# Kernel optimization log

Hardware: AMD Instinct MI355X
Metric: run time of the kernel (lower is better)

## Reference

```python
import jax, jax.numpy as jnp
import numpy as np

N, C = 131072, 1000
ALPHA_LINK = 0.25  # weight applied when pred is a 'linked' (acceptable) confusion of gt
GAMMA = 2.0        # focal exponent


def setup_inputs() -> dict:
    key = jax.random.key(0)
    k1, k2, k3, k4 = jax.random.split(key, 4)
    y_pred = jax.random.normal(k1, (N, C), dtype=jnp.float32)
    y_true = jax.random.randint(k2, (N,), 0, C, dtype=jnp.int64)
    # Dense representation of the python link dict: link_matrix[gt, pred] == True
    # iff pred is in link[gt]; has_link[gt] == True iff gt is a key of link.
    link_matrix = jax.random.bernoulli(k3, 0.01, (C, C))
    has_link = jax.random.bernoulli(k4, 0.5, (C,))
    return {"y_pred": y_pred, "y_true": y_true,
            "link_matrix": link_matrix, "has_link": has_link}


def reference(y_pred, y_true, link_matrix, has_link):
    # per-sample cross entropy (stable log-softmax + gather)
    logp = jax.nn.log_softmax(y_pred, axis=-1)                     # [N, C]
    ce = -jnp.take_along_axis(logp, y_true[:, None], axis=1)[:, 0]  # [N]
    pt = jnp.exp(-ce)                                              # [N]
    pred = jnp.argmax(y_pred, axis=1)                              # [N]
    # link_bad: ALPHA_LINK iff pred != gt, gt in link, and pred in link[gt]; else 1
    linked = link_matrix[y_true, pred] & has_link[y_true] & (pred != y_true)
    w = jnp.where(linked, jnp.float32(ALPHA_LINK), jnp.float32(1.0))
    return jnp.mean(w * (1.0 - pt) ** GAMMA * ce)
```

## Files before the change

### kernel.cpp

```cpp
#include <hip/hip_runtime.h>
#include <math.h>


#define NROWS 131072
#define NC 1000
#define NF4 250
#define ROWS_PER_WAVE 4
#define WAVES_PER_BLOCK 4
#define ROWS_PER_BLOCK (ROWS_PER_WAVE * WAVES_PER_BLOCK)
#define NBLOCKS (NROWS / ROWS_PER_BLOCK)
#define NWAVES (NBLOCKS * WAVES_PER_BLOCK)
#define ALPHA_LINK 0.25f

typedef float floatx4 __attribute__((ext_vector_type(4)));

__device__ __forceinline__ void load_row_nt(const floatx4* __restrict__ rowp,
                                            int lane, floatx4 v[4]) {
    v[0] = __builtin_nontemporal_load(rowp + lane);
    v[1] = __builtin_nontemporal_load(rowp + lane + 64);
    v[2] = __builtin_nontemporal_load(rowp + lane + 128);
    if (lane + 192 < NF4) v[3] = __builtin_nontemporal_load(rowp + lane + 192);
    else                  v[3] = (floatx4){-INFINITY, -INFINITY, -INFINITY, -INFINITY};
}

__device__ __forceinline__ void row_local(const floatx4 v[4], int lane, int tf, int tl,
                                          float& m, int& idx, float& xt, float& s) {
    m = -INFINITY; idx = 1 << 30; xt = 0.0f;
    #pragma unroll
    for (int k = 0; k < 4; ++k) {
        const int f  = lane + 64 * k;
        const int c0 = f * 4;
        const float x0 = v[k].x, x1 = v[k].y, x2 = v[k].z, x3 = v[k].w;
        if (x0 > m) { m = x0; idx = c0; }
        if (x1 > m) { m = x1; idx = c0 + 1; }
        if (x2 > m) { m = x2; idx = c0 + 2; }
        if (x3 > m) { m = x3; idx = c0 + 3; }
        if (f == tf) xt = (tl == 0) ? x0 : (tl == 1) ? x1 : (tl == 2) ? x2 : x3;
    }
    s = 0.0f;
    #pragma unroll
    for (int k = 0; k < 4; ++k) {
        s += __expf(v[k].x - m) + __expf(v[k].y - m)
           + __expf(v[k].z - m) + __expf(v[k].w - m);
    }
}

__global__ __launch_bounds__(256) void lfl_main(
    const float* __restrict__ yp,
    const int* __restrict__ yt,
    const unsigned char* __restrict__ linkb, const int* __restrict__ linki,
    const unsigned char* __restrict__ hasb,  const int* __restrict__ hasi,
    const unsigned int* __restrict__ hlw,
    float* __restrict__ partial)
{
    const int lane  = threadIdx.x & 63;
    const int wid   = threadIdx.x >> 6;
    const int gwave = blockIdx.x * WAVES_PER_BLOCK + wid;

    const int hi = yt[2 * lane + 1];
    const int y64 = (__ballot(hi != 0) == 0ULL);
    const unsigned int h0 = hlw[lane];
    const unsigned int h1 = hlw[lane + 64];
    const unsigned int h2 = hlw[lane + 128];
    const unsigned int h3 = (lane + 192 < NF4) ? hlw[lane + 192] : 0u;
    const int bfmt = (__ballot((h0 > 1u) | (h1 > 1u) | (h2 > 1u) | (h3 > 1u)) != 0ULL);

    const int row0 = blockIdx.x * ROWS_PER_BLOCK + wid * ROWS_PER_WAVE;
    float wsum = 0.0f;

    #pragma unroll
    for (int p = 0; p < ROWS_PER_WAVE / 2; ++p) {
        const int rowA = row0 + 2 * p;
        const int rowB = rowA + 1;

        floatx4 vA[4], vB[4];
        load_row_nt((const floatx4*)(yp + (size_t)rowA * NC), lane, vA);
        load_row_nt((const floatx4*)(yp + (size_t)rowB * NC), lane, vB);

        const int tgtA = y64 ? yt[2 * rowA] : yt[rowA];
        const int tgtB = y64 ? yt[2 * rowB] : yt[rowB];
        const int tfA = tgtA >> 2, tlA = tgtA & 3;
        const int tfB = tgtB >> 2, tlB = tgtB & 3;

        float mA, xtA, sA, mB, xtB, sB;
        int idxA, idxB;
        row_local(vA, lane, tfA, tlA, mA, idxA, xtA, sA);
        row_local(vB, lane, tfB, tlB, mB, idxB, xtB, sB);

        const float xtsA = __shfl(xtA, tfA & 63);
        const float xtsB = __shfl(xtB, tfB & 63);

        #pragma unroll
        for (int off = 32; off; off >>= 1) {
            const float omA = __shfl_xor(mA, off);
            const float omB = __shfl_xor(mB, off);
            const int   oiA = __shfl_xor(idxA, off);
            const int   oiB = __shfl_xor(idxB, off);
            const float osA = __shfl_xor(sA, off);
            const float osB = __shfl_xor(sB, off);
            const float mnA = fmaxf(mA, omA);
            const float mnB = fmaxf(mB, omB);
            sA = sA * __expf(mA - mnA) + osA * __expf(omA - mnA);
            sB = sB * __expf(mB - mnB) + osB * __expf(omB - mnB);
            if (omA > mA || (omA == mA && oiA < idxA)) idxA = oiA;
            if (omB > mB || (omB == mB && oiB < idxB)) idxB = oiB;
            mA = mnA; mB = mnB;
        }

        #pragma unroll
        for (int q = 0; q < 2; ++q) {
            const int   target = q ? tgtB : tgtA;
            const int   pred   = q ? idxB : idxA;
            const float logp_t = (q ? xtsB : xtsA) - (q ? mB : mA) - __logf(q ? sB : sA);
            const float ce = -logp_t;
            const float pt = __expf(logp_t);
            const size_t ofs = (size_t)target * NC + (size_t)pred;
            const bool lm = bfmt ? (linkb[ofs] != 0)   : (linki[ofs] != 0);
            const bool hb = bfmt ? (hasb[target] != 0) : (hasi[target] != 0);
            const float w = (lm && hb && (pred != target)) ? ALPHA_LINK : 1.0f;
            const float ompt = 1.0f - pt;
            wsum += w * ompt * ompt * ce;
        }
    }

    if (lane == 0) partial[gwave] = wsum;
}

__global__ __launch_bounds__(1024) void lfl_final(const float* __restrict__ partial,
                                                  float* __restrict__ out) {
    __shared__ float sm[1024];
    float s = 0.0f;
    for (int i = threadIdx.x; i < NWAVES; i += 1024) s += partial[i];
    sm[threadIdx.x] = s;
    __syncthreads();
    for (int stride = 512; stride; stride >>= 1) {
        if ((int)threadIdx.x < stride) sm[threadIdx.x] += sm[threadIdx.x + stride];
        __syncthreads();
    }
    if (threadIdx.x == 0) out[0] = sm[0] * (1.0f / (float)NROWS);
}

extern "C" void kernel_launch(void* const* d_in, const int* in_sizes, int n_in,
                              void* d_out, int out_size, void* d_ws, size_t ws_size,
                              hipStream_t stream) {
    const float* yp = (const float*)d_in[0];
    const int*   yt = (const int*)d_in[1];
    const void*  lk = d_in[2];
    const void*  hl = d_in[3];

    float* partial = (float*)d_ws;

    lfl_main<<<NBLOCKS, 256, 0, stream>>>(
        yp, yt,
        (const unsigned char*)lk, (const int*)lk,
        (const unsigned char*)hl, (const int*)hl,
        (const unsigned int*)hl,
        partial);
    lfl_final<<<1, 1024, 0, stream>>>(partial, (float*)d_out);
}
```

Before: 103.4 us.

## Double-buffer row-pair loads and process more rows per wave

Cuts the grid to 2048 blocks so each wave handles 16 rows. Row pairs are loaded through two alternating register buffers, so the loads for the next pair are in flight while the current pair computes. Targets are prefetched up front and launch bounds request 4 blocks per CU. This is meant to hide memory latency for a bandwidth-bound kernel, at the cost of higher register pressure and fewer waves to hide latency.

```diff
diff --git a/kernel.cpp b/kernel.cpp
--- a/kernel.cpp
+++ b/kernel.cpp
@@ -5,47 +5,107 @@
 #define NROWS 131072
 #define NC 1000
 #define NF4 250
-#define ROWS_PER_WAVE 4
 #define WAVES_PER_BLOCK 4
-#define ROWS_PER_BLOCK (ROWS_PER_WAVE * WAVES_PER_BLOCK)
-#define NBLOCKS (NROWS / ROWS_PER_BLOCK)
+#define NBLOCKS 2048
 #define NWAVES (NBLOCKS * WAVES_PER_BLOCK)
+#define ROWS_PER_WAVE (NROWS / NWAVES)
+#define NPAIRS (ROWS_PER_WAVE / 2)
 #define ALPHA_LINK 0.25f
 
 typedef float floatx4 __attribute__((ext_vector_type(4)));
 
-__device__ __forceinline__ void load_row_nt(const floatx4* __restrict__ rowp,
-                                            int lane, floatx4 v[4]) {
-    v[0] = __builtin_nontemporal_load(rowp + lane);
-    v[1] = __builtin_nontemporal_load(rowp + lane + 64);
-    v[2] = __builtin_nontemporal_load(rowp + lane + 128);
-    if (lane + 192 < NF4) v[3] = __builtin_nontemporal_load(rowp + lane + 192);
-    else                  v[3] = (floatx4){-INFINITY, -INFINITY, -INFINITY, -INFINITY};
+__device__ __forceinline__ void load_pair_nt(const float* __restrict__ yp,
+                                             int row, int lane, floatx4 v[2][4]) {
+    #pragma unroll
+    for (int r = 0; r < 2; ++r) {
+        const floatx4* rowp = (const floatx4*)(yp + (size_t)(row + r) * NC);
+        v[r][0] = __builtin_nontemporal_load(rowp + lane);
+        v[r][1] = __builtin_nontemporal_load(rowp + lane + 64);
+        v[r][2] = __builtin_nontemporal_load(rowp + lane + 128);
+        if (lane + 192 < NF4) v[r][3] = __builtin_nontemporal_load(rowp + lane + 192);
+        else v[r][3] = (floatx4){-INFINITY, -INFINITY, -INFINITY, -INFINITY};
+    }
 }
 
-__device__ __forceinline__ void row_local(const floatx4 v[4], int lane, int tf, int tl,
-                                          float& m, int& idx, float& xt, float& s) {
-    m = -INFINITY; idx = 1 << 30; xt = 0.0f;
+__device__ __forceinline__ float compute_pair(
+    const floatx4 v[2][4], int lane, int tgtA, int tgtB, int bfmt,
+    const unsigned char* __restrict__ linkb, const int* __restrict__ linki,
+    const unsigned char* __restrict__ hasb,  const int* __restrict__ hasi)
+{
+    const int tfA = tgtA >> 2, tlA = tgtA & 3;
+    const int tfB = tgtB >> 2, tlB = tgtB & 3;
+
+    float mA = -INFINITY, mB = -INFINITY, xtA = 0.0f, xtB = 0.0f;
+    int idxA = 1 << 30, idxB = 1 << 30;
     #pragma unroll
     for (int k = 0; k < 4; ++k) {
         const int f  = lane + 64 * k;
         const int c0 = f * 4;
-        const float x0 = v[k].x, x1 = v[k].y, x2 = v[k].z, x3 = v[k].w;
-        if (x0 > m) { m = x0; idx = c0; }
-        if (x1 > m) { m = x1; idx = c0 + 1; }
-        if (x2 > m) { m = x2; idx = c0 + 2; }
-        if (x3 > m) { m = x3; idx = c0 + 3; }
-        if (f == tf) xt = (tl == 0) ? x0 : (tl == 1) ? x1 : (tl == 2) ? x2 : x3;
+        {
+            const float x0 = v[0][k].x, x1 = v[0][k].y, x2 = v[0][k].z, x3 = v[0][k].w;
+            if (x0 > mA) { mA = x0; idxA = c0; }
+            if (x1 > mA) { mA = x1; idxA = c0 + 1; }
+            if (x2 > mA) { mA = x2; idxA = c0 + 2; }
+            if (x3 > mA) { mA = x3; idxA = c0 + 3; }
+            if (f == tfA) xtA = (tlA == 0) ? x0 : (tlA == 1) ? x1 : (tlA == 2) ? x2 : x3;
+        }
+        {
+            const float x0 = v[1][k].x, x1 = v[1][k].y, x2 = v[1][k].z, x3 = v[1][k].w;
+            if (x0 > mB) { mB = x0; idxB = c0; }
+            if (x1 > mB) { mB = x1; idxB = c0 + 1; }
+            if (x2 > mB) { mB = x2; idxB = c0 + 2; }
+            if (x3 > mB) { mB = x3; idxB = c0 + 3; }
+            if (f == tfB) xtB = (tlB == 0) ? x0 : (tlB == 1) ? x1 : (tlB == 2) ? x2 : x3;
+        }
     }
-    s = 0.0f;
+    float sA = 0.0f, sB = 0.0f;
     #pragma unroll
     for (int k = 0; k < 4; ++k) {
-        s += __expf(v[k].x - m) + __expf(v[k].y - m)
-           + __expf(v[k].z - m) + __expf(v[k].w - m);
+        sA += __expf(v[0][k].x - mA) + __expf(v[0][k].y - mA)
+            + __expf(v[0][k].z - mA) + __expf(v[0][k].w - mA);
+        sB += __expf(v[1][k].x - mB) + __expf(v[1][k].y - mB)
+            + __expf(v[1][k].z - mB) + __expf(v[1][k].w - mB);
     }
+
+    const float xtsA = __shfl(xtA, tfA & 63);
+    const float xtsB = __shfl(xtB, tfB & 63);
+
+    #pragma unroll
+    for (int off = 32; off; off >>= 1) {
+        const float omA = __shfl_xor(mA, off);
+        const float omB = __shfl_xor(mB, off);
+        const int   oiA = __shfl_xor(idxA, off);
+        const int   oiB = __shfl_xor(idxB, off);
+        const float osA = __shfl_xor(sA, off);
+        const float osB = __shfl_xor(sB, off);
+        const float mnA = fmaxf(mA, omA);
+        const float mnB = fmaxf(mB, omB);
+        sA = sA * __expf(mA - mnA) + osA * __expf(omA - mnA);
+        sB = sB * __expf(mB - mnB) + osB * __expf(omB - mnB);
+        if (omA > mA || (omA == mA && oiA < idxA)) idxA = oiA;
+        if (omB > mB || (omB == mB && oiB < idxB)) idxB = oiB;
+        mA = mnA; mB = mnB;
+    }
+
+    float wsum = 0.0f;
+    #pragma unroll
+    for (int q = 0; q < 2; ++q) {
+        const int   target = q ? tgtB : tgtA;
+        const int   pred   = q ? idxB : idxA;
+        const float logp_t = (q ? xtsB : xtsA) - (q ? mB : mA) - __logf(q ? sB : sA);
+        const float ce = -logp_t;
+        const float pt = __expf(logp_t);
+        const size_t ofs = (size_t)target * NC + (size_t)pred;
+        const bool lm = bfmt ? (linkb[ofs] != 0)   : (linki[ofs] != 0);
+        const bool hb = bfmt ? (hasb[target] != 0) : (hasi[target] != 0);
+        const float w = (lm && hb && (pred != target)) ? ALPHA_LINK : 1.0f;
+        const float ompt = 1.0f - pt;
+        wsum += w * ompt * ompt * ce;
+    }
+    return wsum;
 }
 
-__global__ __launch_bounds__(256) void lfl_main(
+__global__ __launch_bounds__(256, 4) void lfl_main(
     const float* __restrict__ yp,
     const int* __restrict__ yt,
     const unsigned char* __restrict__ linkb, const int* __restrict__ linki,
@@ -56,71 +116,40 @@
     const int lane  = threadIdx.x & 63;
     const int wid   = threadIdx.x >> 6;
     const int gwave = blockIdx.x * WAVES_PER_BLOCK + wid;
+    const int row0  = gwave * ROWS_PER_WAVE;
 
-    const int hi = yt[2 * lane + 1];
-    const int y64 = (__ballot(hi != 0) == 0ULL);
+    const int det_hi = yt[2 * lane + 1];
     const unsigned int h0 = hlw[lane];
     const unsigned int h1 = hlw[lane + 64];
     const unsigned int h2 = hlw[lane + 128];
     const unsigned int h3 = (lane + 192 < NF4) ? hlw[lane + 192] : 0u;
+    int t32[ROWS_PER_WAVE], t64[ROWS_PER_WAVE];
+    #pragma unroll
+    for (int r = 0; r < ROWS_PER_WAVE; ++r) {
+        t32[r] = yt[row0 + r];
+        t64[r] = yt[2 * (row0 + r)];
+    }
+
+    floatx4 A[2][4], B[2][4];
+    load_pair_nt(yp, row0, lane, A);
+
+    const int y64  = (__ballot(det_hi != 0) == 0ULL);
     const int bfmt = (__ballot((h0 > 1u) | (h1 > 1u) | (h2 > 1u) | (h3 > 1u)) != 0ULL);
 
-    const int row0 = blockIdx.x * ROWS_PER_BLOCK + wid * ROWS_PER_WAVE;
+    int tgt[ROWS_PER_WAVE];
+    #pragma unroll
+    for (int r = 0; r < ROWS_PER_WAVE; ++r) tgt[r] = y64 ? t64[r] : t32[r];
+
     float wsum = 0.0f;
-
     #pragma unroll
-    for (int p = 0; p < ROWS_PER_WAVE / 2; ++p) {
-        const int rowA = row0 + 2 * p;
-        const int rowB = rowA + 1;
-
-        floatx4 vA[4], vB[4];
-        load_row_nt((const floatx4*)(yp + (size_t)rowA * NC), lane, vA);
-        load_row_nt((const floatx4*)(yp + (size_t)rowB * NC), lane, vB);
-
-        const int tgtA = y64 ? yt[2 * rowA] : yt[rowA];
-        const int tgtB = y64 ? yt[2 * rowB] : yt[rowB];
-        const int tfA = tgtA >> 2, tlA = tgtA & 3;
-        const int tfB = tgtB >> 2, tlB = tgtB & 3;
-
-        float mA, xtA, sA, mB, xtB, sB;
-        int idxA, idxB;
-        row_local(vA, lane, tfA, tlA, mA, idxA, xtA, sA);
-        row_local(vB, lane, tfB, tlB, mB, idxB, xtB, sB);
-
-        const float xtsA = __shfl(xtA, tfA & 63);
-        const float xtsB = __shfl(xtB, tfB & 63);
-
-        #pragma unroll
-        for (int off = 32; off; off >>= 1) {
-            const float omA = __shfl_xor(mA, off);
-            const float omB = __shfl_xor(mB, off);
-            const int   oiA = __shfl_xor(idxA, off);
-            const int   oiB = __shfl_xor(idxB, off);
-            const float osA = __shfl_xor(sA, off);
-            const float osB = __shfl_xor(sB, off);
-            const float mnA = fmaxf(mA, omA);
-            const float mnB = fmaxf(mB, omB);
-            sA = sA * __expf(mA - mnA) + osA * __expf(omA - mnA);
-            sB = sB * __expf(mB - mnB) + osB * __expf(omB - mnB);
-            if (omA > mA || (omA == mA && oiA < idxA)) idxA = oiA;
-            if (omB > mB || (omB == mB && oiB < idxB)) idxB = oiB;
-            mA = mnA; mB = mnB;
-        }
-
-        #pragma unroll
-        for (int q = 0; q < 2; ++q) {
-            const int   target = q ? tgtB : tgtA;
-            const int   pred   = q ? idxB : idxA;
-            const float logp_t = (q ? xtsB : xtsA) - (q ? mB : mA) - __logf(q ? sB : sA);
-            const float ce = -logp_t;
-            const float pt = __expf(logp_t);
-            const size_t ofs = (size_t)target * NC + (size_t)pred;
-            const bool lm = bfmt ? (linkb[ofs] != 0)   : (linki[ofs] != 0);
-            const bool hb = bfmt ? (hasb[target] != 0) : (hasi[target] != 0);
-            const float w = (lm && hb && (pred != target)) ? ALPHA_LINK : 1.0f;
-            const float ompt = 1.0f - pt;
-            wsum += w * ompt * ompt * ce;
-        }
+    for (int p = 0; p < NPAIRS; p += 2) {
+        if (p + 1 < NPAIRS) load_pair_nt(yp, row0 + (p + 1) * 2, lane, B);
+        wsum += compute_pair(A, lane, tgt[2 * p], tgt[2 * p + 1], bfmt,
+                             linkb, linki, hasb, hasi);
+        if (p + 2 < NPAIRS) load_pair_nt(yp, row0 + (p + 2) * 2, lane, A);
+        if (p + 1 < NPAIRS)
+            wsum += compute_pair(B, lane, tgt[2 * p + 2], tgt[2 * p + 3], bfmt,
+                                 linkb, linki, hasb, hasi);
     }
 
     if (lane == 0) partial[gwave] = wsum;
```

New measurement: 179.9 us. 73.9% more time.
